# Kernel optimization log

Measured on AMD Instinct MI355X. Metric: run time of the kernel, lower is better.

## Reference

```python
import jax, jax.numpy as jnp
import numpy as np

BINS = 10
LOSS_WEIGHT = 1.0
EDGE_TOP = 1.0 + 1e-6  # edges[-1] += 1e-6 in the torch module


def setup_inputs() -> dict:
    key = jax.random.key(0)
    k1, k2, k3 = jax.random.split(key, 3)
    shape = (32, 1048576)
    # pred: sigmoid probabilities in [0, 1)
    pred = jax.random.uniform(k1, shape, dtype=jnp.float32)
    target = (jax.random.uniform(k2, shape) < 0.3).astype(jnp.float32)
    label_weight = (jax.random.uniform(k3, shape) < 0.95).astype(jnp.float32)
    return {"pred": pred, "target": target, "label_weight": label_weight}


def reference(pred, target, label_weight):
    p = pred.reshape(-1)
    t = target.reshape(-1).astype(p.dtype)
    lw = label_weight.reshape(-1).astype(p.dtype)

    I = jnp.sum(p * t)                       # intersection
    S = jnp.sum(p) + jnp.sum(t)              # denominator of Dice

    # gradient norm proxy: |2I/S * pred.detach() - target| (no grad flows through g)
    g = jax.lax.stop_gradient(jnp.abs(2.0 * I / S * p - t))

    valid = lw > 0
    tot = jnp.maximum(jnp.sum(valid.astype(p.dtype)), 1.0)

    # bin assignment: edges are i/bins for i=0..bins, with edges[-1] bumped by 1e-6,
    # so g in [i/bins, (i+1)/bins) -> bin i, and g in [1, 1+1e-6) -> bin bins-1.
    in_range = valid & (g < EDGE_TOP)
    bin_idx = jnp.clip(jnp.floor(g * BINS).astype(jnp.int32), 0, BINS - 1)

    # one-pass histogram of valid, in-range elements
    counts = jnp.zeros(BINS, dtype=p.dtype).at[bin_idx].add(in_range.astype(p.dtype))
    n_nonempty = jnp.sum(counts > 0).astype(p.dtype)

    # weight = tot / num_in_bin for elements in a non-empty bin, else 0; then /n
    per_elem = jnp.where(in_range, tot / jnp.maximum(counts[bin_idx], 1.0), 0.0)
    weights = per_elem / jnp.maximum(n_nonempty, 1.0)

    loss = 1.0 - jnp.sum(2.0 * p * t * weights) / S
    return loss * LOSS_WEIGHT
```

## Files before the change

### kernel.cpp

```cpp
#include <hip/hip_runtime.h>


constexpr int BINS   = 10;
constexpr int K      = 4;
constexpr int CH     = 256 * K;
constexpr int BLOCKS = 2048;
constexpr int OFF1   = 64;
constexpr int OFF2   = 16448;
constexpr size_t MASK_OFF = 266240;

template<bool MASK>
__global__ __launch_bounds__(256) void k_pass1(const float4* __restrict__ p,
                                               const float4* __restrict__ t,
                                               const float4* __restrict__ lw,
                                               unsigned char* __restrict__ mask,
                                               float* __restrict__ ws,
                                               int n4, int n) {
    const int tid   = threadIdx.x;
    const int nfull = n4 / CH;
    float sI = 0.f, sP = 0.f, sT = 0.f;

    for (int c = blockIdx.x; c < nfull; c += gridDim.x) {
        const int base = c * CH + tid;
        float4 pv[K], tv[K], wv[K];
#pragma unroll
        for (int k = 0; k < K; ++k) pv[k] = p[base + k * 256];
#pragma unroll
        for (int k = 0; k < K; ++k) tv[k] = t[base + k * 256];
        if constexpr (MASK) {
#pragma unroll
            for (int k = 0; k < K; ++k) wv[k] = lw[base + k * 256];
        }
#pragma unroll
        for (int k = 0; k < K; ++k) {
            sI += pv[k].x * tv[k].x + pv[k].y * tv[k].y + pv[k].z * tv[k].z + pv[k].w * tv[k].w;
            sP += pv[k].x + pv[k].y + pv[k].z + pv[k].w;
            sT += tv[k].x + tv[k].y + tv[k].z + tv[k].w;
            if constexpr (MASK) {
                unsigned int mb = 0;
                mb |= (tv[k].x != 0.f) ? 1u   : 0u;
                mb |= (tv[k].y != 0.f) ? 2u   : 0u;
                mb |= (tv[k].z != 0.f) ? 4u   : 0u;
                mb |= (tv[k].w != 0.f) ? 8u   : 0u;
                mb |= (wv[k].x != 0.f) ? 16u  : 0u;
                mb |= (wv[k].y != 0.f) ? 32u  : 0u;
                mb |= (wv[k].z != 0.f) ? 64u  : 0u;
                mb |= (wv[k].w != 0.f) ? 128u : 0u;
                mask[base + k * 256] = (unsigned char)mb;
            }
        }
    }
    if (blockIdx.x == 0) {
        for (int i = nfull * CH + tid; i < n4; i += 256) {
            float4 pv = p[i], tv = t[i];
            sI += pv.x * tv.x + pv.y * tv.y + pv.z * tv.z + pv.w * tv.w;
            sP += pv.x + pv.y + pv.z + pv.w;
            sT += tv.x + tv.y + tv.z + tv.w;
            if constexpr (MASK) {
                float4 wv = lw[i];
                unsigned int mb = 0;
                mb |= (tv.x != 0.f) ? 1u   : 0u;
                mb |= (tv.y != 0.f) ? 2u   : 0u;
                mb |= (tv.z != 0.f) ? 4u   : 0u;
                mb |= (tv.w != 0.f) ? 8u   : 0u;
                mb |= (wv.x != 0.f) ? 16u  : 0u;
                mb |= (wv.y != 0.f) ? 32u  : 0u;
                mb |= (wv.z != 0.f) ? 64u  : 0u;
                mb |= (wv.w != 0.f) ? 128u : 0u;
                mask[i] = (unsigned char)mb;
            }
        }
        if (tid == 0) {
            const float* pf = (const float*)p;
            const float* tf = (const float*)t;
            for (int i = n4 * 4; i < n; ++i) { sI += pf[i] * tf[i]; sP += pf[i]; sT += tf[i]; }
        }
    }
#pragma unroll
    for (int o = 32; o > 0; o >>= 1) {
        sI += __shfl_down(sI, o);
        sP += __shfl_down(sP, o);
        sT += __shfl_down(sT, o);
    }
    __shared__ float rI[4], rP[4], rT[4];
    int wave = tid >> 6, lane = tid & 63;
    if (lane == 0) { rI[wave] = sI; rP[wave] = sP; rT[wave] = sT; }
    __syncthreads();
    if (tid == 0) {
        float* o = &ws[OFF1 + blockIdx.x * 4];
        o[0] = rI[0] + rI[1] + rI[2] + rI[3];
        o[1] = rP[0] + rP[1] + rP[2] + rP[3];
        o[2] = rT[0] + rT[1] + rT[2] + rT[3];
    }
}

__global__ __launch_bounds__(256) void k_mid(float* __restrict__ ws, int nb1) {
    const float4* pws = (const float4*)&ws[OFF1];
    float aI = 0.f, aP = 0.f, aT = 0.f;
    for (int b = threadIdx.x; b < nb1; b += 256) {
        float4 v = pws[b];
        aI += v.x; aP += v.y; aT += v.z;
    }
    __shared__ float red[256 * 5];
    float* mine = &red[threadIdx.x * 5];
    mine[0] = aI; mine[1] = aP; mine[2] = aT;
    __syncthreads();
    int tid = threadIdx.x;
    if (tid < 3) {
        float s = 0.f;
        for (int i = 0; i < 256; ++i) s += red[i * 5 + tid];
        red[tid] = s;
    }
    __syncthreads();
    if (tid == 0) {
        float I = red[0];
        float S = red[1] + red[2];
        ws[0] = 2.f * I / S;
        ws[1] = S;
    }
}

template<bool MASK>
__global__ __launch_bounds__(256) void k_pass2(const float4* __restrict__ p,
                                               const float4* __restrict__ t,
                                               const float4* __restrict__ lw,
                                               const unsigned char* __restrict__ mask,
                                               float* __restrict__ ws,
                                               int n4, int n) {
    const float scale    = ws[0];
    const float edge_top = 1.0f + 1e-6f;
    const int tid   = threadIdx.x;
    const int nfull = n4 / CH;

    int   cnt[BINS];
    float sm[BINS];
#pragma unroll
    for (int b = 0; b < BINS; ++b) { cnt[b] = 0; sm[b] = 0.f; }
    int vcount = 0;

    auto process = [&](float pe, float te, bool valid) {
        vcount += valid;
        float g = fabsf(scale * pe - te);
        bool inr = valid && (g < edge_top);
        int b = (int)(g * 10.f);
        b = b > (BINS - 1) ? (BINS - 1) : b;
        int slot = inr ? b : BINS;
        float adds = 2.f * pe * te;
#pragma unroll
        for (int b0 = 0; b0 < BINS; ++b0) {
            bool m = (slot == b0);
            cnt[b0] += m;
            sm[b0]  += m ? adds : 0.f;
        }
    };

    for (int c = blockIdx.x; c < nfull; c += gridDim.x) {
        const int base = c * CH + tid;
        float4 pv[K];
#pragma unroll
        for (int k = 0; k < K; ++k) pv[k] = p[base + k * 256];
        if constexpr (MASK) {
            unsigned char mv[K];
#pragma unroll
            for (int k = 0; k < K; ++k) mv[k] = mask[base + k * 256];
#pragma unroll
            for (int k = 0; k < K; ++k) {
                unsigned int m = mv[k];
                process(pv[k].x, (m & 1u)   ? 1.f : 0.f, (m & 16u)  != 0);
                process(pv[k].y, (m & 2u)   ? 1.f : 0.f, (m & 32u)  != 0);
                process(pv[k].z, (m & 4u)   ? 1.f : 0.f, (m & 64u)  != 0);
                process(pv[k].w, (m & 8u)   ? 1.f : 0.f, (m & 128u) != 0);
            }
        } else {
            float4 tv[K], wv[K];
#pragma unroll
            for (int k = 0; k < K; ++k) tv[k] = t[base + k * 256];
#pragma unroll
            for (int k = 0; k < K; ++k) wv[k] = lw[base + k * 256];
#pragma unroll
            for (int k = 0; k < K; ++k) {
                process(pv[k].x, tv[k].x, wv[k].x > 0.f);
                process(pv[k].y, tv[k].y, wv[k].y > 0.f);
                process(pv[k].z, tv[k].z, wv[k].z > 0.f);
                process(pv[k].w, tv[k].w, wv[k].w > 0.f);
            }
        }
    }
    if (blockIdx.x == 0) {
        for (int i = nfull * CH + tid; i < n4; i += 256) {
            float4 pv = p[i], tv = t[i], wv = lw[i];
            process(pv.x, tv.x, wv.x > 0.f);
            process(pv.y, tv.y, wv.y > 0.f);
            process(pv.z, tv.z, wv.z > 0.f);
            process(pv.w, tv.w, wv.w > 0.f);
        }
        if (tid == 0) {
            const float* pf = (const float*)p;
            const float* tf = (const float*)t;
            const float* wf = (const float*)lw;
            for (int i = n4 * 4; i < n; ++i) process(pf[i], tf[i], wf[i] > 0.f);
        }
    }

    __shared__ float red[256 * 21];
    float* mine = &red[tid * 21];
#pragma unroll
    for (int b0 = 0; b0 < BINS; ++b0) {
        mine[b0]        = (float)cnt[b0];
        mine[BINS + b0] = sm[b0];
    }
    mine[2 * BINS] = (float)vcount;
    __syncthreads();

    if (tid < 2 * BINS + 1) {
        float v = 0.f;
        for (int i = 0; i < 256; ++i) v += red[i * 21 + tid];
        ws[OFF2 + blockIdx.x * 24 + tid] = v;
    }
}

__global__ __launch_bounds__(256) void k_final(const float* __restrict__ ws,
                                               float* __restrict__ out, int nb2) {
    float acc[24];
#pragma unroll
    for (int s = 0; s < 24; ++s) acc[s] = 0.f;

    for (int b = threadIdx.x; b < nb2; b += 256) {
        const float4* rec = (const float4*)&ws[OFF2 + b * 24];
        float4 v0 = rec[0], v1 = rec[1], v2 = rec[2],
               v3 = rec[3], v4 = rec[4], v5 = rec[5];
        acc[0]  += v0.x; acc[1]  += v0.y; acc[2]  += v0.z; acc[3]  += v0.w;
        acc[4]  += v1.x; acc[5]  += v1.y; acc[6]  += v1.z; acc[7]  += v1.w;
        acc[8]  += v2.x; acc[9]  += v2.y; acc[10] += v2.z; acc[11] += v2.w;
        acc[12] += v3.x; acc[13] += v3.y; acc[14] += v3.z; acc[15] += v3.w;
        acc[16] += v4.x; acc[17] += v4.y; acc[18] += v4.z; acc[19] += v4.w;
        acc[20] += v5.x;
    }

    __shared__ float red[256 * 25];
    float* mine = &red[threadIdx.x * 25];
#pragma unroll
    for (int s = 0; s <= 2 * BINS; ++s) mine[s] = acc[s];
    __syncthreads();

    __shared__ float fin[24];
    int tid = threadIdx.x;
    if (tid <= 2 * BINS) {
        float s = 0.f;
        for (int i = 0; i < 256; ++i) s += red[i * 25 + tid];
        fin[tid] = s;
    }
    __syncthreads();
    if (tid == 0) {
        float S   = ws[1];
        float tot = fmaxf(fin[20], 1.0f);
        int nne = 0;
        for (int b = 0; b < BINS; ++b) nne += (fin[b] > 0.f) ? 1 : 0;
        float nn = fmaxf((float)nne, 1.0f);
        float wsum = 0.f;
        for (int b = 0; b < BINS; ++b) {
            float c = fmaxf(fin[b], 1.0f);
            wsum += fin[BINS + b] * (tot / c);
        }
        wsum /= nn;
        out[0] = 1.0f - wsum / S;
    }
}

extern "C" void kernel_launch(void* const* d_in, const int* in_sizes, int n_in,
                              void* d_out, int out_size, void* d_ws, size_t ws_size,
                              hipStream_t stream) {
    const float* p  = (const float*)d_in[0];
    const float* t  = (const float*)d_in[1];
    const float* lw = (const float*)d_in[2];
    float* ws  = (float*)d_ws;
    float* out = (float*)d_out;
    int n  = in_sizes[0];
    int n4 = n >> 2;

    unsigned char* mask = (unsigned char*)d_ws + MASK_OFF;
    const bool use_mask = ws_size >= MASK_OFF + (size_t)n4;

    if (use_mask) {
        k_pass1<true><<<BLOCKS, 256, 0, stream>>>((const float4*)p, (const float4*)t,
                                                  (const float4*)lw, mask, ws, n4, n);
        k_mid<<<1, 256, 0, stream>>>(ws, BLOCKS);
        k_pass2<true><<<BLOCKS, 256, 0, stream>>>((const float4*)p, (const float4*)t,
                                                  (const float4*)lw, mask, ws, n4, n);
        k_final<<<1, 256, 0, stream>>>(ws, out, BLOCKS);
    } else {
        k_pass1<false><<<BLOCKS, 256, 0, stream>>>((const float4*)p, (const float4*)t,
                                                   (const float4*)lw, mask, ws, n4, n);
        k_mid<<<1, 256, 0, stream>>>(ws, BLOCKS);
        k_pass2<false><<<BLOCKS, 256, 0, stream>>>((const float4*)p, (const float4*)t,
                                                   (const float4*)lw, mask, ws, n4, n);
        k_final<<<1, 256, 0, stream>>>(ws, out, BLOCKS);
    }
}
```

Baseline: 410.0 us.

## Double-buffer chunk loads in both passes and pack per-thread mask into dwords

Both masked passes now run a two-stage software pipeline: the next chunk's loads are issued before the current chunk is consumed, with scheduling barriers keeping the loads ahead of the arithmetic. The per-element mask bytes for a thread's four float4s are packed into one 32-bit word and stored with a single dword access, replacing four strided byte stores and loads. This aims to hide memory latency and cut narrow memory transactions in a bandwidth-bound kernel. The cost is higher register pressure from holding two buffers of float4 data, which could lower occupancy.

```diff
diff --git a/kernel.cpp b/kernel.cpp
--- a/kernel.cpp
+++ b/kernel.cpp
@@ -9,66 +9,90 @@
 constexpr int OFF2   = 16448;
 constexpr size_t MASK_OFF = 266240;
 
+#define SB0 __builtin_amdgcn_sched_barrier(0)
+
+__device__ __forceinline__ void acc3(const float4& pv, const float4& tv,
+                                     float& sI, float& sP, float& sT) {
+    sI += pv.x * tv.x + pv.y * tv.y + pv.z * tv.z + pv.w * tv.w;
+    sP += pv.x + pv.y + pv.z + pv.w;
+    sT += tv.x + tv.y + tv.z + tv.w;
+}
+
+__device__ __forceinline__ unsigned mbyte(const float4& tv, const float4& wv) {
+    unsigned mb = 0;
+    mb |= (tv.x != 0.f) ? 1u   : 0u;  mb |= (tv.y != 0.f) ? 2u   : 0u;
+    mb |= (tv.z != 0.f) ? 4u   : 0u;  mb |= (tv.w != 0.f) ? 8u   : 0u;
+    mb |= (wv.x != 0.f) ? 16u  : 0u;  mb |= (wv.y != 0.f) ? 32u  : 0u;
+    mb |= (wv.z != 0.f) ? 64u  : 0u;  mb |= (wv.w != 0.f) ? 128u : 0u;
+    return mb;
+}
+
 template<bool MASK>
 __global__ __launch_bounds__(256) void k_pass1(const float4* __restrict__ p,
                                                const float4* __restrict__ t,
                                                const float4* __restrict__ lw,
-                                               unsigned char* __restrict__ mask,
+                                               unsigned* __restrict__ maskw,
                                                float* __restrict__ ws,
                                                int n4, int n) {
     const int tid   = threadIdx.x;
     const int nfull = n4 / CH;
+    const int G     = gridDim.x;
     float sI = 0.f, sP = 0.f, sT = 0.f;
 
-    for (int c = blockIdx.x; c < nfull; c += gridDim.x) {
-        const int base = c * CH + tid;
-        float4 pv[K], tv[K], wv[K];
-#pragma unroll
-        for (int k = 0; k < K; ++k) pv[k] = p[base + k * 256];
-#pragma unroll
-        for (int k = 0; k < K; ++k) tv[k] = t[base + k * 256];
-        if constexpr (MASK) {
-#pragma unroll
-            for (int k = 0; k < K; ++k) wv[k] = lw[base + k * 256];
-        }
-#pragma unroll
-        for (int k = 0; k < K; ++k) {
-            sI += pv[k].x * tv[k].x + pv[k].y * tv[k].y + pv[k].z * tv[k].z + pv[k].w * tv[k].w;
-            sP += pv[k].x + pv[k].y + pv[k].z + pv[k].w;
-            sT += tv[k].x + tv[k].y + tv[k].z + tv[k].w;
-            if constexpr (MASK) {
-                unsigned int mb = 0;
-                mb |= (tv[k].x != 0.f) ? 1u   : 0u;
-                mb |= (tv[k].y != 0.f) ? 2u   : 0u;
-                mb |= (tv[k].z != 0.f) ? 4u   : 0u;
-                mb |= (tv[k].w != 0.f) ? 8u   : 0u;
-                mb |= (wv[k].x != 0.f) ? 16u  : 0u;
-                mb |= (wv[k].y != 0.f) ? 32u  : 0u;
-                mb |= (wv[k].z != 0.f) ? 64u  : 0u;
-                mb |= (wv[k].w != 0.f) ? 128u : 0u;
-                mask[base + k * 256] = (unsigned char)mb;
-            }
-        }
-    }
+    if constexpr (MASK) {
+        float4 Ap[K], At[K], Aw[K], Bp[K], Bt[K], Bw[K];
+
+#define P1_LOAD(P_, T_, W_, c) do { \
+        const int _b = (c) * CH + tid; \
+        _Pragma("unroll") for (int k = 0; k < K; ++k) P_[k] = p[_b + k * 256]; \
+        _Pragma("unroll") for (int k = 0; k < K; ++k) T_[k] = t[_b + k * 256]; \
+        _Pragma("unroll") for (int k = 0; k < K; ++k) W_[k] = lw[_b + k * 256]; \
+    } while (0)
+
+#define P1_CONS(P_, T_, W_, c) do { \
+        _Pragma("unroll") for (int k = 0; k < K; ++k) acc3(P_[k], T_[k], sI, sP, sT); \
+        unsigned mw = mbyte(T_[0], W_[0]) | (mbyte(T_[1], W_[1]) << 8) | \
+                      (mbyte(T_[2], W_[2]) << 16) | (mbyte(T_[3], W_[3]) << 24); \
+        maskw[(c) * 256 + tid] = mw; \
+    } while (0)
+
+        const int bid   = blockIdx.x;
+        const int count = (bid < nfull) ? (nfull - 1 - bid) / G + 1 : 0;
+        if (count > 0) {
+            P1_LOAD(Ap, At, Aw, bid);
+            int j = 0;
+            for (; j + 2 <= count; j += 2) {
+                P1_LOAD(Bp, Bt, Bw, bid + (j + 1) * G);
+                SB0;
+                P1_CONS(Ap, At, Aw, bid + j * G);
+                if (j + 2 < count) P1_LOAD(Ap, At, Aw, bid + (j + 2) * G);
+                SB0;
+                P1_CONS(Bp, Bt, Bw, bid + (j + 1) * G);
+            }
+            if (count & 1) {
+                SB0;
+                P1_CONS(Ap, At, Aw, bid + (count - 1) * G);
+            }
+        }
+#undef P1_LOAD
+#undef P1_CONS
+    } else {
+        for (int c = blockIdx.x; c < nfull; c += G) {
+            const int base = c * CH + tid;
+            float4 pv[K], tv[K];
+#pragma unroll
+            for (int k = 0; k < K; ++k) pv[k] = p[base + k * 256];
+#pragma unroll
+            for (int k = 0; k < K; ++k) tv[k] = t[base + k * 256];
+#pragma unroll
+            for (int k = 0; k < K; ++k) acc3(pv[k], tv[k], sI, sP, sT);
+        }
+    }
+
     if (blockIdx.x == 0) {
         for (int i = nfull * CH + tid; i < n4; i += 256) {
             float4 pv = p[i], tv = t[i];
-            sI += pv.x * tv.x + pv.y * tv.y + pv.z * tv.z + pv.w * tv.w;
-            sP += pv.x + pv.y + pv.z + pv.w;
-            sT += tv.x + tv.y + tv.z + tv.w;
-            if constexpr (MASK) {
-                float4 wv = lw[i];
-                unsigned int mb = 0;
-                mb |= (tv.x != 0.f) ? 1u   : 0u;
-                mb |= (tv.y != 0.f) ? 2u   : 0u;
-                mb |= (tv.z != 0.f) ? 4u   : 0u;
-                mb |= (tv.w != 0.f) ? 8u   : 0u;
-                mb |= (wv.x != 0.f) ? 16u  : 0u;
-                mb |= (wv.y != 0.f) ? 32u  : 0u;
-                mb |= (wv.z != 0.f) ? 64u  : 0u;
-                mb |= (wv.w != 0.f) ? 128u : 0u;
-                mask[i] = (unsigned char)mb;
-            }
+            acc3(pv, tv, sI, sP, sT);
         }
         if (tid == 0) {
             const float* pf = (const float*)p;
@@ -124,13 +148,14 @@
 __global__ __launch_bounds__(256) void k_pass2(const float4* __restrict__ p,
                                                const float4* __restrict__ t,
                                                const float4* __restrict__ lw,
-                                               const unsigned char* __restrict__ mask,
+                                               const unsigned* __restrict__ maskw,
                                                float* __restrict__ ws,
                                                int n4, int n) {
     const float scale    = ws[0];
     const float edge_top = 1.0f + 1e-6f;
     const int tid   = threadIdx.x;
     const int nfull = n4 / CH;
+    const int G     = gridDim.x;
 
     int   cnt[BINS];
     float sm[BINS];
@@ -153,26 +178,54 @@
             sm[b0]  += m ? adds : 0.f;
         }
     };
-
-    for (int c = blockIdx.x; c < nfull; c += gridDim.x) {
-        const int base = c * CH + tid;
-        float4 pv[K];
-#pragma unroll
-        for (int k = 0; k < K; ++k) pv[k] = p[base + k * 256];
-        if constexpr (MASK) {
-            unsigned char mv[K];
-#pragma unroll
-            for (int k = 0; k < K; ++k) mv[k] = mask[base + k * 256];
-#pragma unroll
-            for (int k = 0; k < K; ++k) {
-                unsigned int m = mv[k];
-                process(pv[k].x, (m & 1u)   ? 1.f : 0.f, (m & 16u)  != 0);
-                process(pv[k].y, (m & 2u)   ? 1.f : 0.f, (m & 32u)  != 0);
-                process(pv[k].z, (m & 4u)   ? 1.f : 0.f, (m & 64u)  != 0);
-                process(pv[k].w, (m & 8u)   ? 1.f : 0.f, (m & 128u) != 0);
-            }
-        } else {
-            float4 tv[K], wv[K];
+    auto procq = [&](const float4& q, unsigned b) {
+        process(q.x, (b & 1u) ? 1.f : 0.f, (b & 16u)  != 0);
+        process(q.y, (b & 2u) ? 1.f : 0.f, (b & 32u)  != 0);
+        process(q.z, (b & 4u) ? 1.f : 0.f, (b & 64u)  != 0);
+        process(q.w, (b & 8u) ? 1.f : 0.f, (b & 128u) != 0);
+    };
+
+    if constexpr (MASK) {
+        float4 Ap[K], Bp[K];
+        unsigned Am, Bm;
+
+#define P2_LOAD(P_, M_, c) do { \
+        const int _b = (c) * CH + tid; \
+        _Pragma("unroll") for (int k = 0; k < K; ++k) P_[k] = p[_b + k * 256]; \
+        M_ = maskw[(c) * 256 + tid]; \
+    } while (0)
+
+#define P2_CONS(P_, M_) do { \
+        procq(P_[0], M_);        procq(P_[1], M_ >> 8); \
+        procq(P_[2], M_ >> 16);  procq(P_[3], M_ >> 24); \
+    } while (0)
+
+        const int bid   = blockIdx.x;
+        const int count = (bid < nfull) ? (nfull - 1 - bid) / G + 1 : 0;
+        if (count > 0) {
+            P2_LOAD(Ap, Am, bid);
+            int j = 0;
+            for (; j + 2 <= count; j += 2) {
+                P2_LOAD(Bp, Bm, bid + (j + 1) * G);
+                SB0;
+                P2_CONS(Ap, Am);
+                if (j + 2 < count) P2_LOAD(Ap, Am, bid + (j + 2) * G);
+                SB0;
+                P2_CONS(Bp, Bm);
+            }
+            if (count & 1) {
+                SB0;
+                P2_CONS(Ap, Am);
+            }
+        }
+#undef P2_LOAD
+#undef P2_CONS
+    } else {
+        for (int c = blockIdx.x; c < nfull; c += G) {
+            const int base = c * CH + tid;
+            float4 pv[K], tv[K], wv[K];
+#pragma unroll
+            for (int k = 0; k < K; ++k) pv[k] = p[base + k * 256];
 #pragma unroll
             for (int k = 0; k < K; ++k) tv[k] = t[base + k * 256];
 #pragma unroll
@@ -186,6 +239,7 @@
             }
         }
     }
+
     if (blockIdx.x == 0) {
         for (int i = nfull * CH + tid; i < n4; i += 256) {
             float4 pv = p[i], tv = t[i], wv = lw[i];
@@ -278,22 +332,22 @@
     int n  = in_sizes[0];
     int n4 = n >> 2;
 
-    unsigned char* mask = (unsigned char*)d_ws + MASK_OFF;
+    unsigned* maskw = (unsigned*)((char*)d_ws + MASK_OFF);
     const bool use_mask = ws_size >= MASK_OFF + (size_t)n4;
 
     if (use_mask) {
         k_pass1<true><<<BLOCKS, 256, 0, stream>>>((const float4*)p, (const float4*)t,
-                                                  (const float4*)lw, mask, ws, n4, n);
+                                                  (const float4*)lw, maskw, ws, n4, n);
         k_mid<<<1, 256, 0, stream>>>(ws, BLOCKS);
         k_pass2<true><<<BLOCKS, 256, 0, stream>>>((const float4*)p, (const float4*)t,
-                                                  (const float4*)lw, mask, ws, n4, n);
+                                                  (const float4*)lw, maskw, ws, n4, n);
         k_final<<<1, 256, 0, stream>>>(ws, out, BLOCKS);
     } else {
         k_pass1<false><<<BLOCKS, 256, 0, stream>>>((const float4*)p, (const float4*)t,
-                                                   (const float4*)lw, mask, ws, n4, n);
+                                                   (const float4*)lw, maskw, ws, n4, n);
         k_mid<<<1, 256, 0, stream>>>(ws, BLOCKS);
         k_pass2<false><<<BLOCKS, 256, 0, stream>>>((const float4*)p, (const float4*)t,
-                                                   (const float4*)lw, mask, ws, n4, n);
+                                                   (const float4*)lw, maskw, ws, n4, n);
         k_final<<<1, 256, 0, stream>>>(ws, out, BLOCKS);
     }
 }
```

Measured after the change: 406.5 us. No clear change (-0.8%).
